# Kernel tuning notes

Measured on AMD Instinct MI355X. Metric: run time of the kernel, lower is better.

The kernel has to match this reference:

```python
import jax, jax.numpy as jnp
import numpy as np

N = 50000      # nodes
E = 800000     # edges (avg degree 16)
D_IN = 128
D_H = 256
NUM_LAYERS = 5


def setup_inputs() -> dict:
    key = jax.random.key(0)
    ks = jax.random.split(key, 12)
    s_in = 1.0 / np.sqrt(D_IN)
    s_h = 1.0 / np.sqrt(D_H)
    x = jax.random.normal(ks[0], (N, D_IN), jnp.float32)
    edge_index = jax.random.randint(ks[1], (2, E), 0, N, jnp.int32)
    eps_all = jnp.zeros((NUM_LAYERS,), jnp.float32)
    # torch Linear layout: weight [out, in], y = x @ W.T + b; scaled for stability
    w0_l0 = jax.random.normal(ks[2], (D_H, D_IN), jnp.float32) * s_in
    b0_l0 = jax.random.normal(ks[3], (D_H,), jnp.float32) * 0.01
    w1_l0 = jax.random.normal(ks[4], (D_H, D_H), jnp.float32) * s_h
    b1_l0 = jax.random.normal(ks[5], (D_H,), jnp.float32) * 0.01
    w0_rest = jax.random.normal(ks[6], (4, D_H, D_H), jnp.float32) * s_h
    b0_rest = jax.random.normal(ks[7], (4, D_H), jnp.float32) * 0.01
    w1_rest = jax.random.normal(ks[8], (4, D_H, D_H), jnp.float32) * s_h
    b1_rest = jax.random.normal(ks[9], (4, D_H), jnp.float32) * 0.01
    return {"x": x, "edge_index": edge_index, "eps_all": eps_all,
            "w0_l0": w0_l0, "b0_l0": b0_l0, "w1_l0": w1_l0, "b1_l0": b1_l0,
            "w0_rest": w0_rest, "b0_rest": b0_rest, "w1_rest": w1_rest, "b1_rest": b1_rest}


def _gin_layer(x, src, dst, eps, w0, b0, w1, b1):
    # gather source-node features along edges, scatter-sum into destination nodes
    aggr = jax.ops.segment_sum(x[src], dst, num_segments=N)  # [N, d]
    h = (1.0 + eps) * x + aggr
    h = jax.nn.relu(h @ w0.T + b0)   # dropout p=0.0 -> identity
    h = h @ w1.T + b1
    return jax.nn.relu(h)            # inter-layer ReLU from the trace


def reference(x, edge_index, eps_all, w0_l0, b0_l0, w1_l0, b1_l0,
              w0_rest, b0_rest, w1_rest, b1_rest):
    src = edge_index[0]  # edge_index_j (messages come from row 0)
    dst = edge_index[1]  # edge_index_i (aggregated at row 1)
    h = _gin_layer(x, src, dst, eps_all[0], w0_l0, b0_l0, w1_l0, b1_l0)
    for i in range(4):  # layers 1..4, identical shapes
        h = _gin_layer(h, src, dst, eps_all[i + 1],
                       w0_rest[i], b0_rest[i], w1_rest[i], b1_rest[i])
    return h  # [N, D_H]
```

## Files before the change

kernel.cpp:

```cpp
#include <hip/hip_runtime.h>
#include <hip/hip_bf16.h>
#include <stdint.h>

#define D_IN 128
#define D_H 256
#define NLAYERS 5

typedef __bf16 bf16x8 __attribute__((ext_vector_type(8)));
typedef float f32x4 __attribute__((ext_vector_type(4)));
typedef unsigned short u16x8 __attribute__((ext_vector_type(8)));

__device__ inline unsigned short bfbits(float f) {
  __hip_bfloat16 h = __float2bfloat16(f);
  unsigned short s;
  __builtin_memcpy(&s, &h, 2);
  return s;
}

__device__ inline unsigned packbf(float lo, float hi) {
  return (unsigned)bfbits(lo) | ((unsigned)bfbits(hi) << 16);
}

__device__ inline void addbf2(float& a, float& b, unsigned u) {
  a += __uint_as_float(u << 16);
  b += __uint_as_float(u & 0xffff0000u);
}

__device__ inline void addbf2s(float& a, float& b, unsigned u, float s) {
  a += s * __uint_as_float(u << 16);
  b += s * __uint_as_float(u & 0xffff0000u);
}

__global__ void conv_inputs(const float* __restrict__ x, const float* __restrict__ a,
                            const float* __restrict__ b, const float* __restrict__ c,
                            const float* __restrict__ d,
                            __hip_bfloat16* __restrict__ xb,
                            __hip_bfloat16* __restrict__ wb, int nx) {
  int gid = blockIdx.x * blockDim.x + threadIdx.x;
  if (gid < nx) {
    xb[gid] = __float2bfloat16(x[gid]);
    return;
  }
  gid -= nx;
  if (gid >= 622592) return;
  float v;
  if (gid < 32768) v = a[gid];
  else if (gid < 98304) v = b[gid - 32768];
  else if (gid < 360448) v = c[gid - 98304];
  else v = d[gid - 360448];
  wb[gid] = __float2bfloat16(v);
}

__global__ void zero_ints(int* __restrict__ p, int n) {
  int i = blockIdx.x * blockDim.x + threadIdx.x;
  if (i < n) p[i] = 0;
}

__global__ void hist_kernel(const int* __restrict__ ei, int E, int* __restrict__ deg) {
  int e = blockIdx.x * blockDim.x + threadIdx.x;
  if (e < E) atomicAdd(&deg[ei[E + e]], 1);
}

__global__ __launch_bounds__(256) void block_sums(const int* __restrict__ deg,
                                                  int* __restrict__ bsum, int N) {
  int t = threadIdx.x;
  int idx = blockIdx.x * 1024 + t * 4;
  int4 v = {0, 0, 0, 0};
  if (idx + 3 < N) v = *reinterpret_cast<const int4*>(deg + idx);
  else {
    if (idx + 0 < N) v.x = deg[idx + 0];
    if (idx + 1 < N) v.y = deg[idx + 1];
    if (idx + 2 < N) v.z = deg[idx + 2];
    if (idx + 3 < N) v.w = deg[idx + 3];
  }
  int s = v.x + v.y + v.z + v.w;
#pragma unroll
  for (int off = 32; off > 0; off >>= 1) s += __shfl_down(s, off);
  __shared__ int ws[4];
  int lane = t & 63, w = t >> 6;
  if (lane == 0) ws[w] = s;
  __syncthreads();
  if (t == 0) bsum[blockIdx.x] = ws[0] + ws[1] + ws[2] + ws[3];
}

__global__ void scan_bsums(int* __restrict__ bsum, int nb) {
  int t = threadIdx.x;
  int orig = (t < nb) ? bsum[t] : 0;
  int v = orig;
#pragma unroll
  for (int off = 1; off < 64; off <<= 1) {
    int u = __shfl_up(v, off);
    if (t >= off) v += u;
  }
  if (t < nb) bsum[t] = v - orig;
}

__global__ __launch_bounds__(256) void scan_apply(const int* __restrict__ deg,
                                                  const int* __restrict__ bsum_ex,
                                                  int* __restrict__ row_start, int N) {
  int t = threadIdx.x;
  int idx = blockIdx.x * 1024 + t * 4;
  int4 v = {0, 0, 0, 0};
  if (idx + 3 < N) v = *reinterpret_cast<const int4*>(deg + idx);
  else {
    if (idx + 0 < N) v.x = deg[idx + 0];
    if (idx + 1 < N) v.y = deg[idx + 1];
    if (idx + 2 < N) v.z = deg[idx + 2];
    if (idx + 3 < N) v.w = deg[idx + 3];
  }
  int s = v.x + v.y + v.z + v.w;
  int lane = t & 63, w = t >> 6;
  int sc = s;
#pragma unroll
  for (int off = 1; off < 64; off <<= 1) {
    int u = __shfl_up(sc, off);
    if (lane >= off) sc += u;
  }
  __shared__ int woff[4];
  if (lane == 63) woff[w] = sc;
  __syncthreads();
  int boff = bsum_ex[blockIdx.x];
#pragma unroll
  for (int i = 0; i < 4; ++i)
    if (i < w) boff += woff[i];
  int ex = boff + sc - s;
  if (idx + 3 < N) {
    int4 o;
    o.x = ex;
    o.y = ex + v.x;
    o.z = ex + v.x + v.y;
    o.w = ex + v.x + v.y + v.z;
    *reinterpret_cast<int4*>(row_start + idx) = o;
  } else {
    if (idx + 0 < N) row_start[idx + 0] = ex;
    if (idx + 1 < N) row_start[idx + 1] = ex + v.x;
    if (idx + 2 < N) row_start[idx + 2] = ex + v.x + v.y;
    if (idx + 3 < N) row_start[idx + 3] = ex + v.x + v.y + v.z;
  }
}

__global__ void fill_kernel(const int* __restrict__ ei, int E,
                            const int* __restrict__ row_start,
                            int* __restrict__ cursor, int* __restrict__ csr) {
  int e = blockIdx.x * blockDim.x + threadIdx.x;
  if (e >= E) return;
  int d = ei[E + e];
  int p = atomicAdd(&cursor[d], 1);
  csr[row_start[d] + p] = ei[e];
}

template <int D>
__global__ __launch_bounds__(256) void aggregate(const unsigned short* __restrict__ hb,
                                                 const int* __restrict__ csr,
                                                 const int* __restrict__ row_start,
                                                 const int* __restrict__ deg,
                                                 const float* __restrict__ eps_all,
                                                 int layer,
                                                 unsigned short* __restrict__ pre,
                                                 int N) {
  constexpr int PL = D / 32;
  const int half = threadIdx.x >> 5;
  const int lane = threadIdx.x & 31;
  const int node = blockIdx.x * 8 + half;
  if (node >= N) return;

  const int start = row_start[node];
  const int cnt = deg[node];
  const float epsv = 1.0f + eps_all[layer];

  float acc[PL];
#pragma unroll
  for (int j = 0; j < PL; ++j) acc[j] = 0.0f;

  if (D == 256) {
    uint4 su = *reinterpret_cast<const uint4*>(hb + (size_t)node * D + lane * 8);
    for (int base = 0; base < cnt; base += 32) {
      int m = cnt - base;
      if (m > 32) m = 32;
      int idx = (lane < m) ? csr[start + base + lane] : 0;
      int i = 0;
      for (; i + 8 <= m; i += 8) {
        uint4 q[8];
#pragma unroll
        for (int r = 0; r < 8; ++r) {
          int s = __shfl(idx, i + r, 32);
          q[r] = *reinterpret_cast<const uint4*>(hb + (size_t)s * D + lane * 8);
        }
#pragma unroll
        for (int r = 0; r < 8; ++r) {
          addbf2(acc[0], acc[1], q[r].x);
          addbf2(acc[2], acc[3], q[r].y);
          addbf2(acc[4], acc[5], q[r].z);
          addbf2(acc[6], acc[7], q[r].w);
        }
      }
      for (; i + 4 <= m; i += 4) {
        uint4 q[4];
#pragma unroll
        for (int r = 0; r < 4; ++r) {
          int s = __shfl(idx, i + r, 32);
          q[r] = *reinterpret_cast<const uint4*>(hb + (size_t)s * D + lane * 8);
        }
#pragma unroll
        for (int r = 0; r < 4; ++r) {
          addbf2(acc[0], acc[1], q[r].x);
          addbf2(acc[2], acc[3], q[r].y);
          addbf2(acc[4], acc[5], q[r].z);
          addbf2(acc[6], acc[7], q[r].w);
        }
      }
      for (; i < m; ++i) {
        int s = __shfl(idx, i, 32);
        uint4 q = *reinterpret_cast<const uint4*>(hb + (size_t)s * D + lane * 8);
        addbf2(acc[0], acc[1], q.x);
        addbf2(acc[2], acc[3], q.y);
        addbf2(acc[4], acc[5], q.z);
        addbf2(acc[6], acc[7], q.w);
      }
    }
    addbf2s(acc[0], acc[1], su.x, epsv);
    addbf2s(acc[2], acc[3], su.y, epsv);
    addbf2s(acc[4], acc[5], su.z, epsv);
    addbf2s(acc[6], acc[7], su.w, epsv);
    uint4 o;
    o.x = packbf(acc[0], acc[1]);
    o.y = packbf(acc[2], acc[3]);
    o.z = packbf(acc[4], acc[5]);
    o.w = packbf(acc[6], acc[7]);
    *reinterpret_cast<uint4*>(pre + (size_t)node * D + lane * 8) = o;
  } else {
    uint2 su = *reinterpret_cast<const uint2*>(hb + (size_t)node * D + lane * 4);
    for (int base = 0; base < cnt; base += 32) {
      int m = cnt - base;
      if (m > 32) m = 32;
      int idx = (lane < m) ? csr[start + base + lane] : 0;
      int i = 0;
      for (; i + 8 <= m; i += 8) {
        uint2 q[8];
#pragma unroll
        for (int r = 0; r < 8; ++r) {
          int s = __shfl(idx, i + r, 32);
          q[r] = *reinterpret_cast<const uint2*>(hb + (size_t)s * D + lane * 4);
        }
#pragma unroll
        for (int r = 0; r < 8; ++r) {
          addbf2(acc[0], acc[1], q[r].x);
          addbf2(acc[2], acc[3], q[r].y);
        }
      }
      for (; i + 4 <= m; i += 4) {
        uint2 q[4];
#pragma unroll
        for (int r = 0; r < 4; ++r) {
          int s = __shfl(idx, i + r, 32);
          q[r] = *reinterpret_cast<const uint2*>(hb + (size_t)s * D + lane * 4);
        }
#pragma unroll
        for (int r = 0; r < 4; ++r) {
          addbf2(acc[0], acc[1], q[r].x);
          addbf2(acc[2], acc[3], q[r].y);
        }
      }
      for (; i < m; ++i) {
        int s = __shfl(idx, i, 32);
        uint2 q = *reinterpret_cast<const uint2*>(hb + (size_t)s * D + lane * 4);
        addbf2(acc[0], acc[1], q.x);
        addbf2(acc[2], acc[3], q.y);
      }
    }
    addbf2s(acc[0], acc[1], su.x, epsv);
    addbf2s(acc[2], acc[3], su.y, epsv);
    uint2 o;
    o.x = packbf(acc[0], acc[1]);
    o.y = packbf(acc[2], acc[3]);
    *reinterpret_cast<uint2*>(pre + (size_t)node * D + lane * 4) = o;
  }
}

template <int K, bool OUT_BF16>
__global__ __launch_bounds__(256, 2) void wstat_gemm(
    const unsigned short* __restrict__ Ap, const __hip_bfloat16* __restrict__ Wp,
    const float* __restrict__ bias, void* __restrict__ Outp, int Nrows) {
  constexpr int NK = K / 32;
  const int lane = threadIdx.x & 63;
  const int colgroup = threadIdx.x >> 6;
  const int l15 = lane & 15;
  const int kg = lane >> 4;
  const int col0 = colgroup * 64;

  bf16x8 wfr[NK][4];
  const unsigned short* Ws = (const unsigned short*)Wp;
#pragma unroll
  for (int ct = 0; ct < 4; ++ct) {
    const unsigned short* wrow = Ws + (size_t)(col0 + ct * 16 + l15) * K + kg * 8;
#pragma unroll
    for (int kk = 0; kk < NK; ++kk)
      wfr[kk][ct] = *reinterpret_cast<const bf16x8*>(wrow + kk * 32);
  }
  float bv[4];
#pragma unroll
  for (int ct = 0; ct < 4; ++ct) bv[ct] = bias[col0 + ct * 16 + l15];

  const int nchunks = (Nrows + 31) >> 5;
  for (int c = blockIdx.x; c < nchunks; c += gridDim.x) {
    const int r0 = c << 5;
    bf16x8 afr[NK][2];
#pragma unroll
    for (int rt = 0; rt < 2; ++rt) {
      int row = r0 + rt * 16 + l15;
      if (row > Nrows - 1) row = Nrows - 1;
      const unsigned short* ar = Ap + (size_t)row * K + kg * 8;
#pragma unroll
      for (int kk = 0; kk < NK; ++kk)
        afr[kk][rt] = *reinterpret_cast<const bf16x8*>(ar + kk * 32);
    }
    f32x4 acc[2][4];
#pragma unroll
    for (int rt = 0; rt < 2; ++rt)
#pragma unroll
      for (int ct = 0; ct < 4; ++ct) acc[rt][ct] = 0.0f;
#pragma unroll
    for (int kk = 0; kk < NK; ++kk)
#pragma unroll
      for (int rt = 0; rt < 2; ++rt)
#pragma unroll
        for (int ct = 0; ct < 4; ++ct)
          acc[rt][ct] = __builtin_amdgcn_mfma_f32_16x16x32_bf16(
              afr[kk][rt], wfr[kk][ct], acc[rt][ct], 0, 0, 0);
#pragma unroll
    for (int ct = 0; ct < 4; ++ct) {
      int col = col0 + ct * 16 + l15;
#pragma unroll
      for (int rt = 0; rt < 2; ++rt)
#pragma unroll
        for (int i = 0; i < 4; ++i) {
          int row = r0 + rt * 16 + kg * 4 + i;
          if (row < Nrows) {
            float v = fmaxf(acc[rt][ct][i] + bv[ct], 0.0f);
            if (OUT_BF16)
              ((__hip_bfloat16*)Outp)[(size_t)row * D_H + col] = __float2bfloat16(v);
            else
              ((float*)Outp)[(size_t)row * D_H + col] = v;
          }
        }
    }
  }
}

extern "C" void kernel_launch(void* const* d_in, const int* in_sizes, int n_in,
                              void* d_out, int out_size, void* d_ws, size_t ws_size,
                              hipStream_t stream) {
  const float* x = (const float*)d_in[0];
  const int* ei = (const int*)d_in[1];
  const float* eps_all = (const float*)d_in[2];
  const float* w0_l0 = (const float*)d_in[3];
  const float* b0_l0 = (const float*)d_in[4];
  const float* w1_l0 = (const float*)d_in[5];
  const float* b1_l0 = (const float*)d_in[6];
  const float* w0_rest = (const float*)d_in[7];
  const float* b0_rest = (const float*)d_in[8];
  const float* w1_rest = (const float*)d_in[9];
  const float* b1_rest = (const float*)d_in[10];

  const int N = in_sizes[0] / D_IN;
  const int E = in_sizes[1] / 2;
  const int NX = N * D_IN;

  char* ws = (char*)d_ws;
  const size_t node_bf = (size_t)N * D_H * sizeof(unsigned short);
  unsigned short* h = (unsigned short*)ws;
  unsigned short* pre = (unsigned short*)(ws + node_bf);
  unsigned short* mid = (unsigned short*)(ws + 2 * node_bf);
  unsigned short* xb = (unsigned short*)(ws + 3 * node_bf);
  char* p = ws + 3 * node_bf + (size_t)NX * sizeof(unsigned short);
  __hip_bfloat16* wbf = (__hip_bfloat16*)p;
  p += 622592 * sizeof(__hip_bfloat16);
  int* deg = (int*)p;
  int* cursor = deg + N;
  int* row_start = cursor + N;
  int* bsum = row_start + N;
  int* csr = bsum + 64;

  __hip_bfloat16* w0_l0_bf = wbf;
  __hip_bfloat16* w1_l0_bf = wbf + 32768;
  __hip_bfloat16* w0_rest_bf = wbf + 98304;
  __hip_bfloat16* w1_rest_bf = w0_rest_bf + 262144;

  conv_inputs<<<(NX + 622592 + 255) / 256, 256, 0, stream>>>(
      x, w0_l0, w1_l0, w0_rest, w1_rest, (__hip_bfloat16*)xb, wbf, NX);

  const int nb = (N + 1023) / 1024;
  zero_ints<<<(2 * N + 255) / 256, 256, 0, stream>>>(deg, 2 * N);
  hist_kernel<<<(E + 255) / 256, 256, 0, stream>>>(ei, E, deg);
  block_sums<<<nb, 256, 0, stream>>>(deg, bsum, N);
  scan_bsums<<<1, 64, 0, stream>>>(bsum, nb);
  scan_apply<<<nb, 256, 0, stream>>>(deg, bsum, row_start, N);
  fill_kernel<<<(E + 255) / 256, 256, 0, stream>>>(ei, E, row_start, cursor, csr);

  const int gemmGrid = 512;
  const int aggBlocks = (N + 7) / 8;

  for (int layer = 0; layer < NLAYERS; ++layer) {
    const __hip_bfloat16* w0 =
        (layer == 0) ? w0_l0_bf : w0_rest_bf + (size_t)(layer - 1) * 65536;
    const float* b0 = (layer == 0) ? b0_l0 : b0_rest + (size_t)(layer - 1) * 256;
    const __hip_bfloat16* w1 =
        (layer == 0) ? w1_l0_bf : w1_rest_bf + (size_t)(layer - 1) * 65536;
    const float* b1 = (layer == 0) ? b1_l0 : b1_rest + (size_t)(layer - 1) * 256;

    if (layer == 0) {
      aggregate<D_IN><<<aggBlocks, 256, 0, stream>>>(xb, csr, row_start, deg,
                                                     eps_all, layer, pre, N);
      wstat_gemm<D_IN, true><<<gemmGrid, 256, 0, stream>>>(pre, w0, b0, mid, N);
    } else {
      aggregate<D_H><<<aggBlocks, 256, 0, stream>>>(h, csr, row_start, deg,
                                                    eps_all, layer, pre, N);
      wstat_gemm<D_H, true><<<gemmGrid, 256, 0, stream>>>(pre, w0, b0, mid, N);
    }
    if (layer == NLAYERS - 1)
      wstat_gemm<D_H, false><<<gemmGrid, 256, 0, stream>>>(mid, w1, b1, d_out, N);
    else
      wstat_gemm<D_H, true><<<gemmGrid, 256, 0, stream>>>(mid, w1, b1, h, N);
  }
}
```

Measured before the change: 605.2 us.

## Fuse the two MLP GEMMs per layer with producer/consumer waves via LDS

Replaces the two separate weight-stationary GEMM launches per layer with one fused kernel. Four producer waves compute relu(A·W0ᵀ+b0) for a 32-row chunk into a double-buffered LDS tile, and four consumer waves multiply that tile by W1 and write the output. This removes the global round trip of the intermediate activation and one launch per layer. In exchange the block is larger (512 threads, fewer blocks) with a block-wide barrier per chunk, so producer and consumer stages are lockstepped and occupancy or register pressure may change.

```diff
diff --git a/kernel.cpp b/kernel.cpp
--- a/kernel.cpp
+++ b/kernel.cpp
@@ -9,6 +9,8 @@
 typedef __bf16 bf16x8 __attribute__((ext_vector_type(8)));
 typedef float f32x4 __attribute__((ext_vector_type(4)));
 typedef unsigned short u16x8 __attribute__((ext_vector_type(8)));
+
+#define MID_STRIDE 260
 
 __device__ inline unsigned short bfbits(float f) {
   __hip_bfloat16 h = __float2bfloat16(f);
@@ -277,41 +279,59 @@
   }
 }
 
-template <int K, bool OUT_BF16>
-__global__ __launch_bounds__(256, 2) void wstat_gemm(
-    const unsigned short* __restrict__ Ap, const __hip_bfloat16* __restrict__ Wp,
-    const float* __restrict__ bias, void* __restrict__ Outp, int Nrows) {
-  constexpr int NK = K / 32;
-  const int lane = threadIdx.x & 63;
-  const int colgroup = threadIdx.x >> 6;
+template <int K0, bool OUT_BF16>
+__global__ __launch_bounds__(512, 2) void mlp_fused(
+    const unsigned short* __restrict__ Ap, const __hip_bfloat16* __restrict__ W0p,
+    const float* __restrict__ b0, const __hip_bfloat16* __restrict__ W1p,
+    const float* __restrict__ b1, void* __restrict__ Outp, int Nrows) {
+  __shared__ unsigned short midb[2][32 * MID_STRIDE];
+
+  constexpr int NK0 = K0 / 32;
+  constexpr int NK1 = D_H / 32;
+  const int tid = threadIdx.x;
+  const int wid = tid >> 6;
+  const bool prod = (wid < 4);
+  const int cg = wid & 3;
+  const int lane = tid & 63;
   const int l15 = lane & 15;
   const int kg = lane >> 4;
-  const int col0 = colgroup * 64;
-
-  bf16x8 wfr[NK][4];
-  const unsigned short* Ws = (const unsigned short*)Wp;
-#pragma unroll
-  for (int ct = 0; ct < 4; ++ct) {
-    const unsigned short* wrow = Ws + (size_t)(col0 + ct * 16 + l15) * K + kg * 8;
-#pragma unroll
-    for (int kk = 0; kk < NK; ++kk)
-      wfr[kk][ct] = *reinterpret_cast<const bf16x8*>(wrow + kk * 32);
-  }
+  const int col0 = cg * 64;
+  const int nch = (Nrows + 31) >> 5;
+
+  bf16x8 wfr[NK1][4];
   float bv[4];
-#pragma unroll
-  for (int ct = 0; ct < 4; ++ct) bv[ct] = bias[col0 + ct * 16 + l15];
-
-  const int nchunks = (Nrows + 31) >> 5;
-  for (int c = blockIdx.x; c < nchunks; c += gridDim.x) {
+  if (prod) {
+    const unsigned short* Ws = (const unsigned short*)W0p;
+#pragma unroll
+    for (int ct = 0; ct < 4; ++ct) {
+      const unsigned short* wrow = Ws + (size_t)(col0 + ct * 16 + l15) * K0 + kg * 8;
+#pragma unroll
+      for (int kk = 0; kk < NK0; ++kk)
+        wfr[kk][ct] = *reinterpret_cast<const bf16x8*>(wrow + kk * 32);
+      bv[ct] = b0[col0 + ct * 16 + l15];
+    }
+  } else {
+    const unsigned short* Ws = (const unsigned short*)W1p;
+#pragma unroll
+    for (int ct = 0; ct < 4; ++ct) {
+      const unsigned short* wrow = Ws + (size_t)(col0 + ct * 16 + l15) * D_H + kg * 8;
+#pragma unroll
+      for (int kk = 0; kk < NK1; ++kk)
+        wfr[kk][ct] = *reinterpret_cast<const bf16x8*>(wrow + kk * 32);
+      bv[ct] = b1[col0 + ct * 16 + l15];
+    }
+  }
+
+  auto produce = [&](int c, unsigned short* buf) {
     const int r0 = c << 5;
-    bf16x8 afr[NK][2];
+    bf16x8 afr[NK0][2];
 #pragma unroll
     for (int rt = 0; rt < 2; ++rt) {
       int row = r0 + rt * 16 + l15;
       if (row > Nrows - 1) row = Nrows - 1;
-      const unsigned short* ar = Ap + (size_t)row * K + kg * 8;
-#pragma unroll
-      for (int kk = 0; kk < NK; ++kk)
+      const unsigned short* ar = Ap + (size_t)row * K0 + kg * 8;
+#pragma unroll
+      for (int kk = 0; kk < NK0; ++kk)
         afr[kk][rt] = *reinterpret_cast<const bf16x8*>(ar + kk * 32);
     }
     f32x4 acc[2][4];
@@ -320,13 +340,47 @@
 #pragma unroll
       for (int ct = 0; ct < 4; ++ct) acc[rt][ct] = 0.0f;
 #pragma unroll
-    for (int kk = 0; kk < NK; ++kk)
+    for (int kk = 0; kk < NK0; ++kk)
 #pragma unroll
       for (int rt = 0; rt < 2; ++rt)
 #pragma unroll
         for (int ct = 0; ct < 4; ++ct)
           acc[rt][ct] = __builtin_amdgcn_mfma_f32_16x16x32_bf16(
               afr[kk][rt], wfr[kk][ct], acc[rt][ct], 0, 0, 0);
+#pragma unroll
+    for (int ct = 0; ct < 4; ++ct) {
+      int col = col0 + ct * 16 + l15;
+#pragma unroll
+      for (int rt = 0; rt < 2; ++rt)
+#pragma unroll
+        for (int i = 0; i < 4; ++i) {
+          int row_l = rt * 16 + kg * 4 + i;
+          buf[row_l * MID_STRIDE + col] = bfbits(fmaxf(acc[rt][ct][i] + bv[ct], 0.0f));
+        }
+    }
+  };
+
+  auto consume = [&](int c, const unsigned short* buf) {
+    const int r0 = c << 5;
+    f32x4 acc[2][4];
+#pragma unroll
+    for (int rt = 0; rt < 2; ++rt)
+#pragma unroll
+      for (int ct = 0; ct < 4; ++ct) acc[rt][ct] = 0.0f;
+#pragma unroll
+    for (int kk = 0; kk < NK1; ++kk) {
+      bf16x8 mfr[2];
+#pragma unroll
+      for (int rt = 0; rt < 2; ++rt)
+        mfr[rt] = *reinterpret_cast<const bf16x8*>(
+            buf + (rt * 16 + l15) * MID_STRIDE + kk * 32 + kg * 8);
+#pragma unroll
+      for (int rt = 0; rt < 2; ++rt)
+#pragma unroll
+        for (int ct = 0; ct < 4; ++ct)
+          acc[rt][ct] = __builtin_amdgcn_mfma_f32_16x16x32_bf16(
+              mfr[rt], wfr[kk][ct], acc[rt][ct], 0, 0, 0);
+    }
 #pragma unroll
     for (int ct = 0; ct < 4; ++ct) {
       int col = col0 + ct * 16 + l15;
@@ -344,6 +398,24 @@
           }
         }
     }
+  };
+
+  int c_pr = blockIdx.x;
+  int c_co = blockIdx.x;
+  int pb = 0;
+  if (prod && c_pr < nch) produce(c_pr, midb[0]);
+  __syncthreads();
+  c_pr += gridDim.x;
+  while (c_co < nch) {
+    if (prod) {
+      if (c_pr < nch) produce(c_pr, midb[pb ^ 1]);
+    } else {
+      consume(c_co, midb[pb]);
+    }
+    __syncthreads();
+    pb ^= 1;
+    c_pr += gridDim.x;
+    c_co += gridDim.x;
   }
 }
 
@@ -370,9 +442,8 @@
   const size_t node_bf = (size_t)N * D_H * sizeof(unsigned short);
   unsigned short* h = (unsigned short*)ws;
   unsigned short* pre = (unsigned short*)(ws + node_bf);
-  unsigned short* mid = (unsigned short*)(ws + 2 * node_bf);
-  unsigned short* xb = (unsigned short*)(ws + 3 * node_bf);
-  char* p = ws + 3 * node_bf + (size_t)NX * sizeof(unsigned short);
+  unsigned short* xb = (unsigned short*)(ws + 2 * node_bf);
+  char* p = ws + 2 * node_bf + (size_t)NX * sizeof(unsigned short);
   __hip_bfloat16* wbf = (__hip_bfloat16*)p;
   p += 622592 * sizeof(__hip_bfloat16);
   int* deg = (int*)p;
@@ -397,7 +468,7 @@
   scan_apply<<<nb, 256, 0, stream>>>(deg, bsum, row_start, N);
   fill_kernel<<<(E + 255) / 256, 256, 0, stream>>>(ei, E, row_start, cursor, csr);
 
-  const int gemmGrid = 512;
+  const int mlpGrid = 256;
   const int aggBlocks = (N + 7) / 8;
 
   for (int layer = 0; layer < NLAYERS; ++layer) {
@@ -411,15 +482,15 @@
     if (layer == 0) {
       aggregate<D_IN><<<aggBlocks, 256, 0, stream>>>(xb, csr, row_start, deg,
                                                      eps_all, layer, pre, N);
-      wstat_gemm<D_IN, true><<<gemmGrid, 256, 0, stream>>>(pre, w0, b0, mid, N);
+      mlp_fused<D_IN, true><<<mlpGrid, 512, 0, stream>>>(pre, w0, b0, w1, b1, h, N);
     } else {
       aggregate<D_H><<<aggBlocks, 256, 0, stream>>>(h, csr, row_start, deg,
                                                     eps_all, layer, pre, N);
-      wstat_gemm<D_H, true><<<gemmGrid, 256, 0, stream>>>(pre, w0, b0, mid, N);
-    }
-    if (layer == NLAYERS - 1)
-      wstat_gemm<D_H, false><<<gemmGrid, 256, 0, stream>>>(mid, w1, b1, d_out, N);
-    else
-      wstat_gemm<D_H, true><<<gemmGrid, 256, 0, stream>>>(mid, w1, b1, h, N);
-  }
-}
+      if (layer == NLAYERS - 1)
+        mlp_fused<D_H, false><<<mlpGrid, 512, 0, stream>>>(pre, w0, b0, w1, b1,
+                                                           d_out, N);
+      else
+        mlp_fused<D_H, true><<<mlpGrid, 512, 0, stream>>>(pre, w0, b0, w1, b1, h, N);
+    }
+  }
+}
```

Result: faster. 519.7 us (-14.1%).
